# Kernel tuning notes

Hardware: AMD Instinct MI355X
Metric: run time of the kernel (lower is better)

## Reference

```python
import math
import jax, jax.numpy as jnp
import numpy as np

# --- dimensions ---
B = 32          # crystals
N_PER = 96      # building blocks per crystal
M = B * N_PER   # total nodes = 3072
H = 8           # no_heads
CH = 16         # c_hidden
PQK = 8         # no_qk_points
PV = 12         # no_v_points
CS = 256        # c_s
CZ = 128        # c_z
E = B * N_PER * N_PER  # dense intra-crystal edges = 294912
INV_SOFTPLUS_1 = 0.541324854612918


def _quat_to_rot(q):
    """Unit quaternion [M,4] -> rotation matrices [M,3,3]."""
    w, x, y, z = q[:, 0], q[:, 1], q[:, 2], q[:, 3]
    R = jnp.stack([
        1 - 2 * (y * y + z * z), 2 * (x * y - w * z), 2 * (x * z + w * y),
        2 * (x * y + w * z), 1 - 2 * (x * x + z * z), 2 * (y * z - w * x),
        2 * (x * z - w * y), 2 * (y * z + w * x), 1 - 2 * (x * x + y * y)],
        axis=-1)
    return R.reshape(-1, 3, 3)


def _lin_params(k, din, dout):
    kw, kb = jax.random.split(k)
    W = jax.random.normal(kw, (din, dout), jnp.float32) / np.sqrt(din).astype(np.float32)
    b = jax.random.normal(kb, (dout,), jnp.float32) * 0.01
    return W, b


def setup_inputs() -> dict:
    key = jax.random.key(0)
    ks = jax.random.split(key, 16)
    s = jax.random.normal(ks[0], (M, CS), jnp.float32)
    z = jax.random.normal(ks[1], (E, CZ), jnp.float32)
    quat = jax.random.normal(ks[2], (M, 4), jnp.float32)
    rot = _quat_to_rot(quat / jnp.linalg.norm(quat, axis=-1, keepdims=True))
    trans = jax.random.normal(ks[3], (M, 3), jnp.float32)
    L = jax.random.normal(ks[4], (B, 6), jnp.float32)
    # block-diagonal fully-connected intra-crystal edges
    i = np.repeat(np.arange(N_PER), N_PER)
    j = np.tile(np.arange(N_PER), N_PER)
    off = (np.arange(B) * N_PER)[:, None]
    src = (off + i[None, :]).reshape(-1)
    tgt = (off + j[None, :]).reshape(-1)
    edge_index = jnp.asarray(np.stack([src, tgt]), jnp.int32)
    num_bbs = jnp.full((B,), N_PER, jnp.int32)
    Wq, bq = _lin_params(ks[5], CS, H * CH)
    Wkv, bkv = _lin_params(ks[6], CS, 2 * H * CH)
    Wqp, bqp = _lin_params(ks[7], CS, H * PQK * 3)
    Wkvp, bkvp = _lin_params(ks[8], CS, H * (PQK + PV) * 3)
    Wb, bb = _lin_params(ks[9], CZ, H)
    Wl, bl = _lin_params(ks[10], 6, H)
    head_weights = INV_SOFTPLUS_1 + 0.1 * jax.random.normal(ks[11], (H,), jnp.float32)
    Wout, bout = _lin_params(ks[12], H * (CH + 3 * PV) + 6, CS)
    return dict(s=s, z=z, rot=rot, trans=trans, L=L,
                Wq=Wq, bq=bq, Wkv=Wkv, bkv=bkv, Wqp=Wqp, bqp=bqp,
                Wkvp=Wkvp, bkvp=bkvp, Wb=Wb, bb=bb, Wl=Wl, bl=bl,
                head_weights=head_weights, Wout=Wout, bout=bout,
                edge_index=edge_index, num_bbs=num_bbs)


def reference(s, z, rot, trans, L, Wq, bq, Wkv, bkv, Wqp, bqp, Wkvp, bkvp,
              Wb, bb, Wl, bl, head_weights, Wout, bout, edge_index, num_bbs):
    src, tgt = edge_index[0], edge_index[1]
    # scalar q/k/v
    q = (s @ Wq + bq).reshape(M, H, CH)
    kv = (s @ Wkv + bkv).reshape(M, H, 2 * CH)
    k, v = kv[..., :CH], kv[..., CH:]

    # point q/k/v: torch splits last dim into 3 coord chunks then stacks -> reshape (M,3,H,P)
    def points(W, bias, P):
        p = (s @ W + bias).reshape(M, 3, H, P).transpose(0, 2, 3, 1)  # [M,H,P,3]
        return jnp.einsum('mij,mhpj->mhpi', rot, p) + trans[:, None, None, :]

    q_pts = points(Wqp, bqp, PQK)                 # [M,H,PQK,3] in global frame
    kv_pts = points(Wkvp, bkvp, PQK + PV)         # [M,H,PQK+PV,3]
    k_pts, v_pts = kv_pts[:, :, :PQK], kv_pts[:, :, PQK:]

    b_pair = z @ Wb + bb                          # [E,H]
    batch_idx = jnp.repeat(jnp.arange(B), num_bbs, total_repeat_length=M)  # node -> crystal
    l_nodes = (L @ Wl + bl)[batch_idx]            # [M,H]

    # fused multi-term attention logits
    a = jnp.einsum('ehc,ehc->eh', q[tgt], k[src]) * math.sqrt(1.0 / (4 * CH))
    a = a + 0.5 * b_pair + 0.5 * l_nodes[src]
    disp = q_pts[tgt] - k_pts[src]                # [E,H,PQK,3]
    pt_att = jnp.sum(disp * disp, axis=-1)        # [E,H,PQK]
    hw = jax.nn.softplus(head_weights) * math.sqrt(1.0 / (4 * (PQK * 9.0 / 2)))
    a = a - 0.5 * jnp.sum(pt_att * hw[None, :, None], axis=-1)

    # segment softmax over incoming edges of each target node
    amax = jax.ops.segment_max(a, tgt, num_segments=M)
    ex = jnp.exp(a - amax[tgt])
    denom = jax.ops.segment_sum(ex, tgt, num_segments=M)
    attn = ex / denom[tgt]                        # [E,H]

    o = jax.ops.segment_sum(attn[..., None] * v[src], tgt, num_segments=M)
    o = o.reshape(M, H * CH)
    o_pt = jax.ops.segment_sum(attn[..., None, None] * v_pts[src], tgt, num_segments=M)
    o_pt = o_pt.reshape(M, H * PV, 3)
    o_l = L[batch_idx]                            # [M,6]
    o_feats = jnp.concatenate([o, o_pt[..., 0], o_pt[..., 1], o_pt[..., 2], o_l], axis=-1)
    return o_feats @ Wout + bout                  # [M,CS]
```

## Files before the change

kernel.cpp:

```cpp
#include <hip/hip_runtime.h>
#include <math.h>

#define B_    32
#define NPER_ 96
#define M_    3072
#define H_    8
#define CH_   16
#define PQK_  8
#define PV_   12
#define CS_   256
#define CZ_   128
#define E_    294912
#define NCAT_ 1056
#define OF_   432

template <bool ALIGN_A>
__global__ __launch_bounds__(256) void gemm64(const float* __restrict__ A,
                                              const float* __restrict__ W,
                                              const float* __restrict__ bias,
                                              float* __restrict__ C,
                                              int N, int K, int KW) {
  __shared__ float As[16][68];
  __shared__ float Bs[16][64];
  const int tid = threadIdx.x;
  const int tx = tid & 15, ty = tid >> 4;
  const int row0 = blockIdx.y * 64, col0 = blockIdx.x * 64;
  float acc[4][4] = {};

  for (int k0 = 0; k0 < K; k0 += 16) {
    {
      const int m = tid >> 2, k4 = (tid & 3) * 4;
      const int gk = k0 + k4;
      float a0 = 0.f, a1 = 0.f, a2 = 0.f, a3 = 0.f;
      if (ALIGN_A) {
        const float4 av = *reinterpret_cast<const float4*>(A + (size_t)(row0 + m) * K + gk);
        a0 = av.x; a1 = av.y; a2 = av.z; a3 = av.w;
      } else {
        const float* ap = A + (size_t)(row0 + m) * K;
        if (gk + 0 < K) a0 = ap[gk + 0];
        if (gk + 1 < K) a1 = ap[gk + 1];
        if (gk + 2 < K) a2 = ap[gk + 2];
        if (gk + 3 < K) a3 = ap[gk + 3];
      }
      As[k4 + 0][m] = a0; As[k4 + 1][m] = a1; As[k4 + 2][m] = a2; As[k4 + 3][m] = a3;
    }
    {
      const int kk = tid >> 4, n4 = (tid & 15) * 4;
      const int gk = k0 + kk, gn = col0 + n4;
      float4 bv; bv.x = 0.f; bv.y = 0.f; bv.z = 0.f; bv.w = 0.f;
      if (gk < KW) {
        if (gn + 3 < N) {
          bv = *reinterpret_cast<const float4*>(W + (size_t)gk * N + gn);
        } else {
          const float* wp = W + (size_t)gk * N;
          if (gn + 0 < N) bv.x = wp[gn + 0];
          if (gn + 1 < N) bv.y = wp[gn + 1];
          if (gn + 2 < N) bv.z = wp[gn + 2];
          if (gn + 3 < N) bv.w = wp[gn + 3];
        }
      }
      *reinterpret_cast<float4*>(&Bs[kk][n4]) = bv;
    }
    __syncthreads();
#pragma unroll
    for (int kk = 0; kk < 16; ++kk) {
      const float4 a_ = *reinterpret_cast<const float4*>(&As[kk][ty * 4]);
      const float4 b_ = *reinterpret_cast<const float4*>(&Bs[kk][tx * 4]);
      acc[0][0] += a_.x * b_.x; acc[0][1] += a_.x * b_.y; acc[0][2] += a_.x * b_.z; acc[0][3] += a_.x * b_.w;
      acc[1][0] += a_.y * b_.x; acc[1][1] += a_.y * b_.y; acc[1][2] += a_.y * b_.z; acc[1][3] += a_.y * b_.w;
      acc[2][0] += a_.z * b_.x; acc[2][1] += a_.z * b_.y; acc[2][2] += a_.z * b_.z; acc[2][3] += a_.z * b_.w;
      acc[3][0] += a_.w * b_.x; acc[3][1] += a_.w * b_.y; acc[3][2] += a_.w * b_.z; acc[3][3] += a_.w * b_.w;
    }
    __syncthreads();
  }
  const int gn0 = col0 + tx * 4;
#pragma unroll
  for (int i2 = 0; i2 < 4; ++i2) {
    const int gr = row0 + ty * 4 + i2;
    if (gn0 + 3 < N) {
      const float4 bsv = *reinterpret_cast<const float4*>(bias + gn0);
      float4 cv;
      cv.x = acc[i2][0] + bsv.x; cv.y = acc[i2][1] + bsv.y;
      cv.z = acc[i2][2] + bsv.z; cv.w = acc[i2][3] + bsv.w;
      *reinterpret_cast<float4*>(C + (size_t)gr * N + gn0) = cv;
    } else {
#pragma unroll
      for (int j2 = 0; j2 < 4; ++j2) {
        const int gn = gn0 + j2;
        if (gn < N) C[(size_t)gr * N + gn] = acc[i2][j2] + bias[gn];
      }
    }
  }
}

__global__ __launch_bounds__(256) void pack_w(const float* __restrict__ Wq,
                                              const float* __restrict__ Wkv,
                                              const float* __restrict__ Wqp,
                                              const float* __restrict__ Wkvp,
                                              const float* __restrict__ bq,
                                              const float* __restrict__ bkv,
                                              const float* __restrict__ bqp,
                                              const float* __restrict__ bkvp,
                                              float* __restrict__ Wcat,
                                              float* __restrict__ bcat) {
  const int t = blockIdx.x * 256 + threadIdx.x;
  if (t < 256 * NCAT_) {
    const int k = t / NCAT_, n = t - k * NCAT_;
    float v;
    if (n < 128)      v = Wq [k * 128 + n];
    else if (n < 384) v = Wkv[k * 256 + n - 128];
    else if (n < 576) v = Wqp[k * 192 + n - 384];
    else              v = Wkvp[k * 480 + n - 576];
    Wcat[t] = v;
  }
  if (t < NCAT_) {
    float v;
    if (t < 128)      v = bq[t];
    else if (t < 384) v = bkv[t - 128];
    else if (t < 576) v = bqp[t - 384];
    else              v = bkvp[t - 576];
    bcat[t] = v;
  }
}

__global__ __launch_bounds__(256) void rotate_pts(const float* __restrict__ praw,
                                                  const float* __restrict__ rot,
                                                  const float* __restrict__ trans,
                                                  const float* __restrict__ L,
                                                  float* __restrict__ qpts,
                                                  float* __restrict__ kpts,
                                                  float* __restrict__ vpts,
                                                  float* __restrict__ ofeat) {
  const int m = blockIdx.x;
  const int t = threadIdx.x;
  float R[9], T[3];
#pragma unroll
  for (int a = 0; a < 9; ++a) R[a] = rot[m * 9 + a];
#pragma unroll
  for (int a = 0; a < 3; ++a) T[a] = trans[m * 3 + a];
  const float* prow = praw + (size_t)m * NCAT_;

  if (t < 64) {
    const float x = prow[384 + t];
    const float y = prow[384 + 64 + t];
    const float z = prow[384 + 128 + t];
    const int h = t >> 3, p = t & 7;
    float* dst = qpts + ((size_t)(m * 8 + h) * 8 + p) * 3;
    dst[0] = R[0] * x + R[1] * y + R[2] * z + T[0];
    dst[1] = R[3] * x + R[4] * y + R[5] * z + T[1];
    dst[2] = R[6] * x + R[7] * y + R[8] * z + T[2];
  } else if (t < 224) {
    const int idx = t - 64;
    const float x = prow[576 + idx];
    const float y = prow[576 + 160 + idx];
    const float z = prow[576 + 320 + idx];
    const int h = idx / 20, p = idx % 20;
    const float o0 = R[0] * x + R[1] * y + R[2] * z + T[0];
    const float o1 = R[3] * x + R[4] * y + R[5] * z + T[1];
    const float o2 = R[6] * x + R[7] * y + R[8] * z + T[2];
    float* dst = (p < 8) ? (kpts + ((size_t)(m * 8 + h) * 8 + p) * 3)
                         : (vpts + ((size_t)(m * 8 + h) * 12 + (p - 8)) * 3);
    dst[0] = o0; dst[1] = o1; dst[2] = o2;
  } else if (t < 230) {
    ofeat[(size_t)m * OF_ + 416 + (t - 224)] = L[(m / NPER_) * 6 + (t - 224)];
  }
}

__global__ __launch_bounds__(256) void bpair_kernel(const float* __restrict__ z,
                                                    const float* __restrict__ Wb,
                                                    const float* __restrict__ bb,
                                                    float* __restrict__ bT2) {
  __shared__ float lds_out[96 * 9];
  const int bid = blockIdx.x;
  const int b = bid / 96, j = bid - b * 96;
  const int l = threadIdx.x & 63;
  const int w = threadIdx.x >> 6;
  const float4* W4 = reinterpret_cast<const float4*>(Wb);
  const float4 w0 = W4[l * 4 + 0];
  const float4 w1 = W4[l * 4 + 1];
  const float4 w2 = W4[l * 4 + 2];
  const float4 w3 = W4[l * 4 + 3];
  const int b0 = l & 1, b1 = (l >> 1) & 1, b2 = (l >> 2) & 1;
  const int myh = (b0 << 2) | (b1 << 1) | b2;
  const float mybb = bb[myh];
  const float2* z2 = reinterpret_cast<const float2*>(z);

#pragma unroll 1
  for (int i = w; i < 96; i += 4) {
    const size_t e = (size_t)b * 9216 + (size_t)i * 96 + j;
    const float2 zv = z2[e * 64 + l];
    float a0 = zv.x * w0.x + zv.y * w2.x;
    float a1 = zv.x * w0.y + zv.y * w2.y;
    float a2 = zv.x * w0.z + zv.y * w2.z;
    float a3 = zv.x * w0.w + zv.y * w2.w;
    float a4 = zv.x * w1.x + zv.y * w3.x;
    float a5 = zv.x * w1.y + zv.y * w3.y;
    float a6 = zv.x * w1.z + zv.y * w3.z;
    float a7 = zv.x * w1.w + zv.y * w3.w;
    float s40 = (b0 ? a4 : a0) + __shfl_xor(b0 ? a0 : a4, 1);
    float s41 = (b0 ? a5 : a1) + __shfl_xor(b0 ? a1 : a5, 1);
    float s42 = (b0 ? a6 : a2) + __shfl_xor(b0 ? a2 : a6, 1);
    float s43 = (b0 ? a7 : a3) + __shfl_xor(b0 ? a3 : a7, 1);
    float s20 = (b1 ? s42 : s40) + __shfl_xor(b1 ? s40 : s42, 2);
    float s21 = (b1 ? s43 : s41) + __shfl_xor(b1 ? s41 : s43, 2);
    float s1 = (b2 ? s21 : s20) + __shfl_xor(b2 ? s20 : s21, 4);
    s1 += __shfl_xor(s1, 8);
    s1 += __shfl_xor(s1, 16);
    s1 += __shfl_xor(s1, 32);
    if (l < 8) lds_out[i * 9 + myh] = s1 + mybb;
  }
  __syncthreads();
  for (int idx = threadIdx.x; idx < 768; idx += 256) {
    const int h = idx / 96, i = idx - h * 96;
    bT2[(size_t)h * E_ + (size_t)b * 9216 + j * 96 + i] = lds_out[i * 9 + h];
  }
}

__global__ __launch_bounds__(384, 3) void attn_kernel(const float* __restrict__ praw,
                                                      const float* __restrict__ qpts,
                                                      const float* __restrict__ kpts,
                                                      const float* __restrict__ vpts,
                                                      const float* __restrict__ bT2,
                                                      const float* __restrict__ L,
                                                      const float* __restrict__ Wl,
                                                      const float* __restrict__ bl,
                                                      const float* __restrict__ hwts,
                                                      float* __restrict__ ofeat) {
  const int bid = blockIdx.x;
  const int b = bid >> 4, h = (bid >> 1) & 7, half = bid & 1;
  const int j0 = half * 48;
  __shared__ float4 k4[96 * 5];
  __shared__ float4 v4[96 * 5];
  __shared__ float4 kp4[96 * 6];
  __shared__ float4 vp4[96 * 9];
  __shared__ float lds_b[48 * 100];
  const int tid = threadIdx.x;

  for (int t = tid; t < 96 * 8; t += 384) {
    const int i = t >> 3, c = t & 7;
    const float4* src = reinterpret_cast<const float4*>(praw + (size_t)(b * 96 + i) * NCAT_ + 128 + h * 32);
    if (c < 4) k4[i * 5 + c] = src[c];
    else       v4[i * 5 + (c - 4)] = src[c];
  }
  for (int t = tid; t < 96 * 6; t += 384) {
    const int i = t / 6, c = t - i * 6;
    kp4[t] = reinterpret_cast<const float4*>(kpts + ((size_t)(b * 96 + i) * 8 + h) * 24)[c];
  }
  for (int t = tid; t < 96 * 9; t += 384) {
    const int i = t / 9, c = t - i * 9;
    vp4[t] = reinterpret_cast<const float4*>(vpts + ((size_t)(b * 96 + i) * 8 + h) * 36)[c];
  }
  {
    const float4* g4 = reinterpret_cast<const float4*>(bT2 + (size_t)h * E_ + (size_t)b * 9216 + (size_t)j0 * 96);
    for (int t = tid; t < 48 * 24; t += 384) {
      const int jj = t / 24, c = t - jj * 24;
      reinterpret_cast<float4*>(lds_b + jj * 100)[c] = g4[t];
    }
  }
  __syncthreads();

  const int jl = tid >> 3, qq = tid & 7;
  const int j = j0 + jl;
  const int mj = b * 96 + j;

  float lb = bl[h];
#pragma unroll
  for (int d = 0; d < 6; ++d) lb += L[b * 6 + d] * Wl[d * 8 + h];
  const float c_l = 0.5f * lb;
  const float sp = logf(1.0f + __expf(hwts[h]));
  const float c_pt = 0.5f * sp * (1.0f / 12.0f);

  const float4* q4 = reinterpret_cast<const float4*>(praw + (size_t)mj * NCAT_ + h * 16);
  const float4 qa = q4[0], qb = q4[1], qc = q4[2], qd = q4[3];
  float qp[24];
  {
    const float4* qp4 = reinterpret_cast<const float4*>(qpts + ((size_t)mj * 8 + h) * 24);
#pragma unroll
    for (int c4 = 0; c4 < 6; ++c4) {
      const float4 v_ = qp4[c4];
      qp[c4 * 4 + 0] = v_.x; qp[c4 * 4 + 1] = v_.y; qp[c4 * 4 + 2] = v_.z; qp[c4 * 4 + 3] = v_.w;
    }
  }

  float lg[12];
  float mx = -3.0e38f;
#pragma unroll
  for (int s = 0; s < 12; ++s) {
    const int i = s * 8 + qq;
    const float4 ka = k4[i * 5 + 0], kb = k4[i * 5 + 1], kc = k4[i * 5 + 2], kd = k4[i * 5 + 3];
    float dot = qa.x * ka.x + qa.y * ka.y + qa.z * ka.z + qa.w * ka.w
              + qb.x * kb.x + qb.y * kb.y + qb.z * kb.z + qb.w * kb.w
              + qc.x * kc.x + qc.y * kc.y + qc.z * kc.z + qc.w * kc.w
              + qd.x * kd.x + qd.y * kd.y + qd.z * kd.z + qd.w * kd.w;
    float pd = 0.f;
#pragma unroll
    for (int c4 = 0; c4 < 6; ++c4) {
      const float4 kp = kp4[i * 6 + c4];
      const float d0 = qp[c4 * 4 + 0] - kp.x;
      const float d1 = qp[c4 * 4 + 1] - kp.y;
      const float d2 = qp[c4 * 4 + 2] - kp.z;
      const float d3 = qp[c4 * 4 + 3] - kp.w;
      pd += d0 * d0 + d1 * d1 + d2 * d2 + d3 * d3;
    }
    const float lv = dot * 0.125f + 0.5f * lds_b[jl * 100 + i] + c_l - c_pt * pd;
    lg[s] = lv;
    mx = fmaxf(mx, lv);
  }
  mx = fmaxf(mx, __shfl_xor(mx, 1));
  mx = fmaxf(mx, __shfl_xor(mx, 2));
  mx = fmaxf(mx, __shfl_xor(mx, 4));
  float sum = 0.f;
#pragma unroll
  for (int s = 0; s < 12; ++s) { lg[s] = __expf(lg[s] - mx); sum += lg[s]; }
  sum += __shfl_xor(sum, 1);
  sum += __shfl_xor(sum, 2);
  sum += __shfl_xor(sum, 4);
  const float inv = 1.0f / sum;

  float acco[16] = {};
  float accp[36] = {};
#pragma unroll
  for (int s = 0; s < 12; ++s) {
    const int i = s * 8 + qq;
    const float w = lg[s];
#pragma unroll
    for (int c4 = 0; c4 < 4; ++c4) {
      const float4 vv = v4[i * 5 + c4];
      acco[c4 * 4 + 0] += w * vv.x; acco[c4 * 4 + 1] += w * vv.y;
      acco[c4 * 4 + 2] += w * vv.z; acco[c4 * 4 + 3] += w * vv.w;
    }
#pragma unroll
    for (int c4 = 0; c4 < 9; ++c4) {
      const float4 pv = vp4[i * 9 + c4];
      accp[c4 * 4 + 0] += w * pv.x; accp[c4 * 4 + 1] += w * pv.y;
      accp[c4 * 4 + 2] += w * pv.z; accp[c4 * 4 + 3] += w * pv.w;
    }
  }
#pragma unroll
  for (int u = 0; u < 16; ++u) {
    acco[u] += __shfl_xor(acco[u], 1); acco[u] += __shfl_xor(acco[u], 2); acco[u] += __shfl_xor(acco[u], 4);
  }
#pragma unroll
  for (int u = 0; u < 36; ++u) {
    accp[u] += __shfl_xor(accp[u], 1); accp[u] += __shfl_xor(accp[u], 2); accp[u] += __shfl_xor(accp[u], 4);
  }

  if (qq == 0) {
    float* orow = ofeat + (size_t)mj * OF_;
#pragma unroll
    for (int c = 0; c < 16; ++c) orow[h * 16 + c] = acco[c] * inv;
#pragma unroll
    for (int d = 0; d < 3; ++d)
#pragma unroll
      for (int p = 0; p < 12; ++p)
        orow[128 + d * 96 + h * 12 + p] = accp[p * 3 + d] * inv;
  }
}

extern "C" void kernel_launch(void* const* d_in, const int* in_sizes, int n_in,
                              void* d_out, int out_size, void* d_ws, size_t ws_size,
                              hipStream_t stream) {
  const float* s     = (const float*)d_in[0];
  const float* z     = (const float*)d_in[1];
  const float* rot   = (const float*)d_in[2];
  const float* trans = (const float*)d_in[3];
  const float* L     = (const float*)d_in[4];
  const float* Wq    = (const float*)d_in[5];
  const float* bq    = (const float*)d_in[6];
  const float* Wkv   = (const float*)d_in[7];
  const float* bkv   = (const float*)d_in[8];
  const float* Wqp   = (const float*)d_in[9];
  const float* bqp   = (const float*)d_in[10];
  const float* Wkvp  = (const float*)d_in[11];
  const float* bkvp  = (const float*)d_in[12];
  const float* Wb    = (const float*)d_in[13];
  const float* bb    = (const float*)d_in[14];
  const float* Wl    = (const float*)d_in[15];
  const float* bl    = (const float*)d_in[16];
  const float* hwts  = (const float*)d_in[17];
  const float* Wout  = (const float*)d_in[18];
  const float* bout  = (const float*)d_in[19];
  float* out = (float*)d_out;
  float* ws  = (float*)d_ws;

  float* praw  = ws;
  float* qpts  = praw  + 3244032;
  float* kpts  = qpts  + 589824;
  float* vpts  = kpts  + 589824;
  float* ofeat = vpts  + 884736;
  float* bT2   = ofeat + 1327104;
  float* Wcat  = bT2   + 2359296;
  float* bcat  = Wcat  + 270336;

  pack_w<<<(256 * NCAT_ + 255) / 256, 256, 0, stream>>>(Wq, Wkv, Wqp, Wkvp, bq, bkv, bqp, bkvp, Wcat, bcat);
  gemm64<true ><<<dim3(17, 48), 256, 0, stream>>>(s, Wcat, bcat, praw, NCAT_, 256, 256);
  rotate_pts<<<M_, 256, 0, stream>>>(praw, rot, trans, L, qpts, kpts, vpts, ofeat);
  bpair_kernel<<<B_ * NPER_, 256, 0, stream>>>(z, Wb, bb, bT2);
  attn_kernel<<<512, 384, 0, stream>>>(praw, qpts, kpts, vpts, bT2, L, Wl, bl, hwts, ofeat);
  gemm64<true ><<<dim3(4, 48), 256, 0, stream>>>(ofeat, Wout, bout, out, 256, OF_, 422);
}
```

Baseline: 379.8 us.

## Use 128-row GEMM tile, contiguous bpair z reads, and whole-crystal attention blocks

Adds a gemm128 kernel with 128x64 tiles for the input projection, which halves the row-block count and increases register reuse. bpair now has each block read a contiguous source row of z (coalesced per block) and writes bT2 in natural [h][i][j] order. Attention instead reads the bias transposed from LDS and uses one 768-thread block per (crystal, head) rather than two half blocks. The larger attention block needs more LDS and registers per block, which may lower occupancy and leaves only 256 blocks in the grid.

```diff
diff --git a/kernel.cpp b/kernel.cpp
--- a/kernel.cpp
+++ b/kernel.cpp
@@ -77,6 +77,78 @@
 #pragma unroll
   for (int i2 = 0; i2 < 4; ++i2) {
     const int gr = row0 + ty * 4 + i2;
+    if (gn0 + 3 < N) {
+      const float4 bsv = *reinterpret_cast<const float4*>(bias + gn0);
+      float4 cv;
+      cv.x = acc[i2][0] + bsv.x; cv.y = acc[i2][1] + bsv.y;
+      cv.z = acc[i2][2] + bsv.z; cv.w = acc[i2][3] + bsv.w;
+      *reinterpret_cast<float4*>(C + (size_t)gr * N + gn0) = cv;
+    } else {
+#pragma unroll
+      for (int j2 = 0; j2 < 4; ++j2) {
+        const int gn = gn0 + j2;
+        if (gn < N) C[(size_t)gr * N + gn] = acc[i2][j2] + bias[gn];
+      }
+    }
+  }
+}
+
+__global__ __launch_bounds__(256) void gemm128(const float* __restrict__ A,
+                                               const float* __restrict__ W,
+                                               const float* __restrict__ bias,
+                                               float* __restrict__ C,
+                                               int N, int K) {
+  __shared__ float As[16][132];
+  __shared__ float Bs[16][64];
+  const int tid = threadIdx.x;
+  const int tx = tid & 15, ty = tid >> 4;
+  const int row0 = blockIdx.y * 128, col0 = blockIdx.x * 64;
+  float acc[8][4] = {};
+
+  for (int k0 = 0; k0 < K; k0 += 16) {
+#pragma unroll
+    for (int u = 0; u < 2; ++u) {
+      const int idx = tid * 2 + u;
+      const int r = idx >> 2, c = (idx & 3) * 4;
+      const float4 av = *reinterpret_cast<const float4*>(A + (size_t)(row0 + r) * K + k0 + c);
+      As[c + 0][r] = av.x; As[c + 1][r] = av.y; As[c + 2][r] = av.z; As[c + 3][r] = av.w;
+    }
+    {
+      const int kk = tid >> 4, n4 = (tid & 15) * 4;
+      const int gn = col0 + n4;
+      float4 bv; bv.x = 0.f; bv.y = 0.f; bv.z = 0.f; bv.w = 0.f;
+      if (gn + 3 < N) {
+        bv = *reinterpret_cast<const float4*>(W + (size_t)(k0 + kk) * N + gn);
+      } else {
+        const float* wp = W + (size_t)(k0 + kk) * N;
+        if (gn + 0 < N) bv.x = wp[gn + 0];
+        if (gn + 1 < N) bv.y = wp[gn + 1];
+        if (gn + 2 < N) bv.z = wp[gn + 2];
+        if (gn + 3 < N) bv.w = wp[gn + 3];
+      }
+      *reinterpret_cast<float4*>(&Bs[kk][n4]) = bv;
+    }
+    __syncthreads();
+#pragma unroll
+    for (int kk = 0; kk < 16; ++kk) {
+      const float4 a0 = *reinterpret_cast<const float4*>(&As[kk][ty * 8]);
+      const float4 a1 = *reinterpret_cast<const float4*>(&As[kk][ty * 8 + 4]);
+      const float4 b_ = *reinterpret_cast<const float4*>(&Bs[kk][tx * 4]);
+      acc[0][0] += a0.x * b_.x; acc[0][1] += a0.x * b_.y; acc[0][2] += a0.x * b_.z; acc[0][3] += a0.x * b_.w;
+      acc[1][0] += a0.y * b_.x; acc[1][1] += a0.y * b_.y; acc[1][2] += a0.y * b_.z; acc[1][3] += a0.y * b_.w;
+      acc[2][0] += a0.z * b_.x; acc[2][1] += a0.z * b_.y; acc[2][2] += a0.z * b_.z; acc[2][3] += a0.z * b_.w;
+      acc[3][0] += a0.w * b_.x; acc[3][1] += a0.w * b_.y; acc[3][2] += a0.w * b_.z; acc[3][3] += a0.w * b_.w;
+      acc[4][0] += a1.x * b_.x; acc[4][1] += a1.x * b_.y; acc[4][2] += a1.x * b_.z; acc[4][3] += a1.x * b_.w;
+      acc[5][0] += a1.y * b_.x; acc[5][1] += a1.y * b_.y; acc[5][2] += a1.y * b_.z; acc[5][3] += a1.y * b_.w;
+      acc[6][0] += a1.z * b_.x; acc[6][1] += a1.z * b_.y; acc[6][2] += a1.z * b_.z; acc[6][3] += a1.z * b_.w;
+      acc[7][0] += a1.w * b_.x; acc[7][1] += a1.w * b_.y; acc[7][2] += a1.w * b_.z; acc[7][3] += a1.w * b_.w;
+    }
+    __syncthreads();
+  }
+  const int gn0 = col0 + tx * 4;
+#pragma unroll
+  for (int i2 = 0; i2 < 8; ++i2) {
+    const int gr = row0 + ty * 8 + i2;
     if (gn0 + 3 < N) {
       const float4 bsv = *reinterpret_cast<const float4*>(bias + gn0);
       float4 cv;
@@ -172,7 +244,7 @@
                                                     float* __restrict__ bT2) {
   __shared__ float lds_out[96 * 9];
   const int bid = blockIdx.x;
-  const int b = bid / 96, j = bid - b * 96;
+  const int b = bid / 96, i = bid - b * 96;
   const int l = threadIdx.x & 63;
   const int w = threadIdx.x >> 6;
   const float4* W4 = reinterpret_cast<const float4*>(Wb);
@@ -184,11 +256,11 @@
   const int myh = (b0 << 2) | (b1 << 1) | b2;
   const float mybb = bb[myh];
   const float2* z2 = reinterpret_cast<const float2*>(z);
+  const size_t e0 = (size_t)b * 9216 + (size_t)i * 96;
 
 #pragma unroll 1
-  for (int i = w; i < 96; i += 4) {
-    const size_t e = (size_t)b * 9216 + (size_t)i * 96 + j;
-    const float2 zv = z2[e * 64 + l];
+  for (int j = w; j < 96; j += 4) {
+    const float2 zv = z2[(e0 + j) * 64 + l];
     float a0 = zv.x * w0.x + zv.y * w2.x;
     float a1 = zv.x * w0.y + zv.y * w2.y;
     float a2 = zv.x * w0.z + zv.y * w2.z;
@@ -207,16 +279,16 @@
     s1 += __shfl_xor(s1, 8);
     s1 += __shfl_xor(s1, 16);
     s1 += __shfl_xor(s1, 32);
-    if (l < 8) lds_out[i * 9 + myh] = s1 + mybb;
+    if (l < 8) lds_out[j * 9 + myh] = s1 + mybb;
   }
   __syncthreads();
   for (int idx = threadIdx.x; idx < 768; idx += 256) {
-    const int h = idx / 96, i = idx - h * 96;
-    bT2[(size_t)h * E_ + (size_t)b * 9216 + j * 96 + i] = lds_out[i * 9 + h];
-  }
-}
-
-__global__ __launch_bounds__(384, 3) void attn_kernel(const float* __restrict__ praw,
+    const int h = idx / 96, j = idx - h * 96;
+    bT2[(size_t)h * E_ + e0 + j] = lds_out[j * 9 + h];
+  }
+}
+
+__global__ __launch_bounds__(768, 3) void attn_kernel(const float* __restrict__ praw,
                                                       const float* __restrict__ qpts,
                                                       const float* __restrict__ kpts,
                                                       const float* __restrict__ vpts,
@@ -226,41 +298,38 @@
                                                       const float* __restrict__ bl,
                                                       const float* __restrict__ hwts,
                                                       float* __restrict__ ofeat) {
-  const int bid = blockIdx.x;
-  const int b = bid >> 4, h = (bid >> 1) & 7, half = bid & 1;
-  const int j0 = half * 48;
+  const int b = blockIdx.x >> 3, h = blockIdx.x & 7;
   __shared__ float4 k4[96 * 5];
   __shared__ float4 v4[96 * 5];
   __shared__ float4 kp4[96 * 6];
   __shared__ float4 vp4[96 * 9];
-  __shared__ float lds_b[48 * 100];
+  __shared__ float lds_b[96 * 100];
   const int tid = threadIdx.x;
 
-  for (int t = tid; t < 96 * 8; t += 384) {
-    const int i = t >> 3, c = t & 7;
+  {
+    const int i = tid >> 3, c = tid & 7;
     const float4* src = reinterpret_cast<const float4*>(praw + (size_t)(b * 96 + i) * NCAT_ + 128 + h * 32);
     if (c < 4) k4[i * 5 + c] = src[c];
     else       v4[i * 5 + (c - 4)] = src[c];
   }
-  for (int t = tid; t < 96 * 6; t += 384) {
+  for (int t = tid; t < 96 * 6; t += 768) {
     const int i = t / 6, c = t - i * 6;
     kp4[t] = reinterpret_cast<const float4*>(kpts + ((size_t)(b * 96 + i) * 8 + h) * 24)[c];
   }
-  for (int t = tid; t < 96 * 9; t += 384) {
+  for (int t = tid; t < 96 * 9; t += 768) {
     const int i = t / 9, c = t - i * 9;
     vp4[t] = reinterpret_cast<const float4*>(vpts + ((size_t)(b * 96 + i) * 8 + h) * 36)[c];
   }
   {
-    const float4* g4 = reinterpret_cast<const float4*>(bT2 + (size_t)h * E_ + (size_t)b * 9216 + (size_t)j0 * 96);
-    for (int t = tid; t < 48 * 24; t += 384) {
-      const int jj = t / 24, c = t - jj * 24;
-      reinterpret_cast<float4*>(lds_b + jj * 100)[c] = g4[t];
+    const float4* g4 = reinterpret_cast<const float4*>(bT2 + (size_t)h * E_ + (size_t)b * 9216);
+    for (int t = tid; t < 2304; t += 768) {
+      const int ii = t / 24, c = t - ii * 24;
+      reinterpret_cast<float4*>(lds_b + ii * 100)[c] = g4[t];
     }
   }
   __syncthreads();
 
-  const int jl = tid >> 3, qq = tid & 7;
-  const int j = j0 + jl;
+  const int j = tid >> 3, qq = tid & 7;
   const int mj = b * 96 + j;
 
   float lb = bl[h];
@@ -302,7 +371,7 @@
       const float d3 = qp[c4 * 4 + 3] - kp.w;
       pd += d0 * d0 + d1 * d1 + d2 * d2 + d3 * d3;
     }
-    const float lv = dot * 0.125f + 0.5f * lds_b[jl * 100 + i] + c_l - c_pt * pd;
+    const float lv = dot * 0.125f + 0.5f * lds_b[i * 100 + j] + c_l - c_pt * pd;
     lg[s] = lv;
     mx = fmaxf(mx, lv);
   }
@@ -393,9 +462,9 @@
   float* bcat  = Wcat  + 270336;
 
   pack_w<<<(256 * NCAT_ + 255) / 256, 256, 0, stream>>>(Wq, Wkv, Wqp, Wkvp, bq, bkv, bqp, bkvp, Wcat, bcat);
-  gemm64<true ><<<dim3(17, 48), 256, 0, stream>>>(s, Wcat, bcat, praw, NCAT_, 256, 256);
+  gemm128<<<dim3(17, 24), 256, 0, stream>>>(s, Wcat, bcat, praw, NCAT_, 256);
   rotate_pts<<<M_, 256, 0, stream>>>(praw, rot, trans, L, qpts, kpts, vpts, ofeat);
-  bpair_kernel<<<B_ * NPER_, 256, 0, stream>>>(z, Wb, bb, bT2);
-  attn_kernel<<<512, 384, 0, stream>>>(praw, qpts, kpts, vpts, bT2, L, Wl, bl, hwts, ofeat);
+  bpair_kernel<<<M_, 256, 0, stream>>>(z, Wb, bb, bT2);
+  attn_kernel<<<256, 768, 0, stream>>>(praw, qpts, kpts, vpts, bT2, L, Wl, bl, hwts, ofeat);
   gemm64<true ><<<dim3(4, 48), 256, 0, stream>>>(ofeat, Wout, bout, out, 256, OF_, 422);
 }
```

Measured after the change: 387.4 us. 1.02x slower.
